# Optimization experiments

Hardware: AMD Instinct MI355X
Metric: run time of the kernel (lower is better)

The kernel has to match this reference:

```python
import jax, jax.numpy as jnp
import numpy as np

B, S, D, H = 2, 2048, 2048, 16
HD = D // H
DFF = 4 * D
EPS = 1e-5


def _gelu(x):
    # tanh-approximate GELU as in the torch module
    c = jnp.sqrt(jnp.asarray(2.0 / jnp.pi, dtype=x.dtype))
    return 0.5 * x * (1.0 + jnp.tanh(c * (x + 0.044715 * x ** 3)))


def _layernorm(x, scale, shift):
    mean = jnp.mean(x, axis=-1, keepdims=True)
    var = jnp.mean((x - mean) ** 2, axis=-1, keepdims=True)  # unbiased=False
    return scale * (x - mean) / jnp.sqrt(var + EPS) + shift


def setup_inputs() -> dict:
    key = jax.random.key(0)
    ks = jax.random.split(key, 8)
    std = 0.02
    return {
        "x": jax.random.normal(ks[0], (B, S, D), dtype=jnp.float32),
        "Wq": std * jax.random.normal(ks[1], (D, D), dtype=jnp.float32),
        "Wk": std * jax.random.normal(ks[2], (D, D), dtype=jnp.float32),
        "Wv": std * jax.random.normal(ks[3], (D, D), dtype=jnp.float32),
        "Wo": std * jax.random.normal(ks[4], (D, D), dtype=jnp.float32),
        "bo": jnp.zeros((D,), dtype=jnp.float32),
        "ln1_scale": jnp.ones((D,), dtype=jnp.float32),
        "ln1_shift": jnp.zeros((D,), dtype=jnp.float32),
        "ln2_scale": jnp.ones((D,), dtype=jnp.float32),
        "ln2_shift": jnp.zeros((D,), dtype=jnp.float32),
        "W1": std * jax.random.normal(ks[5], (D, DFF), dtype=jnp.float32),
        "b1": jnp.zeros((DFF,), dtype=jnp.float32),
        "W2": std * jax.random.normal(ks[6], (DFF, D), dtype=jnp.float32),
        "b2": jnp.zeros((D,), dtype=jnp.float32),
    }


def _attention(x, Wq, Wk, Wv, Wo, bo):
    b, s, d = x.shape
    q = (x @ Wq).reshape(b, s, H, HD).transpose(0, 2, 1, 3)  # bhsd
    k = (x @ Wk).reshape(b, s, H, HD).transpose(0, 2, 1, 3)
    v = (x @ Wv).reshape(b, s, H, HD).transpose(0, 2, 1, 3)
    scores = jnp.einsum("bhqd,bhkd->bhqk", q, k)
    causal = jnp.tril(jnp.ones((s, s), dtype=bool))
    scores = jnp.where(causal, scores, -jnp.inf)
    w = jax.nn.softmax(scores / jnp.sqrt(jnp.asarray(HD, dtype=x.dtype)), axis=-1)
    ctx = jnp.einsum("bhqk,bhkd->bhqd", w, v)
    ctx = ctx.transpose(0, 2, 1, 3).reshape(b, s, d)
    return ctx @ Wo + bo


def reference(x, Wq, Wk, Wv, Wo, bo, ln1_scale, ln1_shift, ln2_scale, ln2_shift, W1, b1, W2, b2):
    # pre-LN transformer block; dropout rate 0 -> identity
    h = x + _attention(_layernorm(x, ln1_scale, ln1_shift), Wq, Wk, Wv, Wo, bo)
    y = _gelu(_layernorm(h, ln2_scale, ln2_shift) @ W1 + b1)
    return h + (y @ W2 + b2)
```

## Files before the change

### kernel.cpp

```cpp
#include <hip/hip_runtime.h>
#include <cmath>


typedef unsigned short u16;
typedef unsigned int   u32;
typedef float  f32x4   __attribute__((ext_vector_type(4)));
typedef short  s16x8   __attribute__((ext_vector_type(8)));
typedef short  s16x4   __attribute__((ext_vector_type(4)));
typedef __bf16 bf16x8  __attribute__((ext_vector_type(8)));

#define DEV __device__ __forceinline__

DEV u16 f2bf(float f) {
  union { float f; u32 u; } v; v.f = f;
  u32 u = v.u;
  u += 0x7fffu + ((u >> 16) & 1u);
  return (u16)(u >> 16);
}

DEV f32x4 mfma16(s16x8 a, s16x8 b, f32x4 c) {
  return __builtin_amdgcn_mfma_f32_16x16x32_bf16(
      __builtin_bit_cast(bf16x8, a), __builtin_bit_cast(bf16x8, b), c, 0, 0, 0);
}

DEV float gelu_f(float x) {
  const float c = 0.7978845608028654f;
  const float z = c * (x + 0.044715f * x * x * x);
  const float e = __expf(2.0f * z);
  const float th = 1.0f - 2.0f / (e + 1.0f);
  return 0.5f * x * (1.0f + th);
}

DEV void gload16(const u16* g, u16* l) {
  __builtin_amdgcn_global_load_lds(
      (const __attribute__((address_space(1))) u32*)(const void*)g,
      (__attribute__((address_space(3))) u32*)(void*)l, 16, 0, 0);
}

__global__ __launch_bounds__(256) void transpose_cast(
    const float* __restrict__ W, u16* __restrict__ Wt, int K, int N) {
  __shared__ float tile[32][33];
  const int n0 = blockIdx.x * 32, k0 = blockIdx.y * 32;
  const int tx = threadIdx.x, ty = threadIdx.y;
#pragma unroll
  for (int i = 0; i < 4; ++i)
    tile[ty + 8 * i][tx] = W[(size_t)(k0 + ty + 8 * i) * N + n0 + tx];
  __syncthreads();
#pragma unroll
  for (int i = 0; i < 4; ++i)
    Wt[(size_t)(n0 + ty + 8 * i) * K + k0 + tx] = f2bf(tile[tx][ty + 8 * i]);
}

__global__ __launch_bounds__(256) void transpose_v(
    const u16* __restrict__ QKV, u16* __restrict__ VT) {
  __shared__ u16 tile[32][33];
  const int s0 = blockIdx.x * 32;
  const int d0 = blockIdx.y * 32;
  const int bh = blockIdx.z;
  const int b = bh >> 4, h = bh & 15;
  const int tx = threadIdx.x, ty = threadIdx.y;
  const u16* src = QKV + (long)b * 2048 * 6144 + 4096 + h * 128;
#pragma unroll
  for (int i = 0; i < 4; ++i)
    tile[ty + 8 * i][tx] = src[(long)(s0 + ty + 8 * i) * 6144 + d0 + tx];
  __syncthreads();
  u16* dst = VT + (long)bh * 128 * 2048;
#pragma unroll
  for (int i = 0; i < 4; ++i)
    dst[(long)(d0 + ty + 8 * i) * 2048 + s0 + tx] = tile[tx][ty + 8 * i];
}

__global__ __launch_bounds__(256) void ln_kernel(
    const float* __restrict__ X, const float* __restrict__ sc,
    const float* __restrict__ sh, u16* __restrict__ Y) {
  const int row = blockIdx.x, t = threadIdx.x;
  const float* xr = X + (size_t)row * 2048;
  float4 v0 = ((const float4*)xr)[t];
  float4 v1 = ((const float4*)xr)[t + 256];
  float s  = v0.x + v0.y + v0.z + v0.w + v1.x + v1.y + v1.z + v1.w;
  float qs = v0.x*v0.x + v0.y*v0.y + v0.z*v0.z + v0.w*v0.w
           + v1.x*v1.x + v1.y*v1.y + v1.z*v1.z + v1.w*v1.w;
#pragma unroll
  for (int off = 1; off < 64; off <<= 1) {
    s  += __shfl_xor(s, off);
    qs += __shfl_xor(qs, off);
  }
  __shared__ float rs[4], rq[4];
  if ((t & 63) == 0) { rs[t >> 6] = s; rq[t >> 6] = qs; }
  __syncthreads();
  const float st = rs[0] + rs[1] + rs[2] + rs[3];
  const float qt = rq[0] + rq[1] + rq[2] + rq[3];
  const float mean = st * (1.0f / 2048.0f);
  const float var  = qt * (1.0f / 2048.0f) - mean * mean;
  const float rstd = rsqrtf(var + 1e-5f);

  u16* yr = Y + (size_t)row * 2048;
  const int c0 = t * 4, c1 = 1024 + t * 4;
  s16x4 o0, o1;
  o0[0] = (short)f2bf(sc[c0+0] * (v0.x - mean) * rstd + sh[c0+0]);
  o0[1] = (short)f2bf(sc[c0+1] * (v0.y - mean) * rstd + sh[c0+1]);
  o0[2] = (short)f2bf(sc[c0+2] * (v0.z - mean) * rstd + sh[c0+2]);
  o0[3] = (short)f2bf(sc[c0+3] * (v0.w - mean) * rstd + sh[c0+3]);
  o1[0] = (short)f2bf(sc[c1+0] * (v1.x - mean) * rstd + sh[c1+0]);
  o1[1] = (short)f2bf(sc[c1+1] * (v1.y - mean) * rstd + sh[c1+1]);
  o1[2] = (short)f2bf(sc[c1+2] * (v1.z - mean) * rstd + sh[c1+2]);
  o1[3] = (short)f2bf(sc[c1+3] * (v1.w - mean) * rstd + sh[c1+3]);
  *(s16x4*)(yr + c0) = o0;
  *(s16x4*)(yr + c1) = o1;
}

template<int MHALF, int STORE_BF16, int BIAS, int RES, int GELU_ACT>
__global__ __launch_bounds__(512, 2) void gemm8(
    const u16* __restrict__ A, const u16* __restrict__ Bt,
    const float* __restrict__ bias, const float* __restrict__ res,
    float* __restrict__ Cf, u16* __restrict__ Cb,
    int M, int N, int K, int rr, int rc) {
  constexpr int NPH   = 2 * MHALF;
  constexpr int ABUFS = (MHALF == 2) ? 2 : 3;
  constexpr int ASZ   = 8192 * MHALF;
  constexpr int BOFF  = ABUFS * ASZ;
  __shared__ u16 lds[BOFF + 2 * 16384];

  const int t9 = threadIdx.x;
  const int l = t9 & 63, w = t9 >> 6;
  const int r16 = l & 15, quad = l >> 4;
  const int wm = w >> 2, wn = w & 3;

  const int nbx = N >> 8;
  const int bid = blockIdx.x;
  const int xcd = bid & 7, j = bid >> 3;
  const int nregc = nbx / rc;
  const int m_t = (xcd / nregc) * rr + (j % rr);
  const int n_t = (xcd % nregc) * rc + (j / rr);
  const long m0 = (long)m_t * (128 * MHALF);
  const long n0 = (long)n_t * 256;

  const int NT = K >> 6;
  const int srow = t9 >> 3;
  const int scol = (t9 & 7) ^ (srow & 7);

  const u16* Abase = A  + (m0 + srow) * (long)K + scol * 8;
  const u16* Bbase = Bt + (n0 + srow) * (long)K + scol * 8;
  const long rowK64  = 64 * (long)K;
  const long rowK128 = 128 * (long)K;

  #define STAGE_A(tile, h) { \
    u16* d = &lds[((tile) % ABUFS) * ASZ + (h) * 8192 + w * 512]; \
    const u16* s = Abase + (h) * rowK128 + (long)(tile) * 64; \
    gload16(s, d); gload16(s + rowK64, d + 4096); }
  #define STAGE_B(tile, h) { \
    u16* d = &lds[BOFF + ((tile) & 1) * 16384 + (h) * 8192 + w * 512]; \
    const u16* s = Bbase + (h) * rowK128 + (long)(tile) * 64; \
    gload16(s, d); gload16(s + rowK64, d + 4096); }

  f32x4 acc[4 * MHALF][4] = {};

  if (MHALF == 2) {
    STAGE_B(0, 0); STAGE_B(0, 1); STAGE_A(0, 0); STAGE_A(0, 1);
    STAGE_B(1, 0); STAGE_B(1, 1);
    asm volatile("s_waitcnt vmcnt(4)" ::: "memory");
  } else {
    STAGE_B(0, 0); STAGE_B(0, 1); STAGE_A(0, 0); STAGE_A(1, 0);
    STAGE_B(1, 0); STAGE_B(1, 1);
    asm volatile("s_waitcnt vmcnt(6)" ::: "memory");
  }
  __builtin_amdgcn_sched_barrier(0);
  __builtin_amdgcn_s_barrier();

  s16x8 bf_[4][2];
  for (int t = 0; t < NT; ++t) {
    const int ab = t % ABUFS;
    const u16* Abuf = &lds[ab * ASZ];
    const u16* Bbuf = &lds[BOFF + (t & 1) * 16384];
#pragma unroll
    for (int p = 0; p < NPH; ++p) {
      if (p == 0) {
#pragma unroll
        for (int ni = 0; ni < 4; ++ni) {
          const int brow = wn * 64 + ni * 16 + r16;
#pragma unroll
          for (int ks = 0; ks < 2; ++ks)
            bf_[ni][ks] = *(const s16x8*)&Bbuf[brow * 64 + ((ks * 4 + quad) ^ (brow & 7)) * 8];
        }
      }
      s16x8 af[2][2];
#pragma unroll
      for (int mi = 0; mi < 2; ++mi) {
        const int arow = (MHALF == 2 ? wm * 128 : wm * 64) + (2 * p + mi) * 16 + r16;
#pragma unroll
        for (int ks = 0; ks < 2; ++ks)
          af[mi][ks] = *(const s16x8*)&Abuf[arow * 64 + ((ks * 4 + quad) ^ (arow & 7)) * 8];
      }
      if (MHALF == 2) {
        if (p < 2)       { if (t + 1 < NT) STAGE_A(t + 1, p); }
        else             { if (t + 2 < NT) STAGE_B(t + 2, p - 2); }
      } else {
        if (p == 0)      { if (t + 2 < NT) STAGE_A(t + 2, 0); }
        else             { if (t + 2 < NT) { STAGE_B(t + 2, 0); STAGE_B(t + 2, 1); } }
      }
      __builtin_amdgcn_sched_barrier(0);
      __builtin_amdgcn_s_barrier();
      asm volatile("s_waitcnt lgkmcnt(0)" ::: "memory");
      __builtin_amdgcn_sched_barrier(0);
      __builtin_amdgcn_s_setprio(1);
#pragma unroll
      for (int mi = 0; mi < 2; ++mi)
#pragma unroll
        for (int ni = 0; ni < 4; ++ni)
#pragma unroll
          for (int ks = 0; ks < 2; ++ks)
            acc[2 * p + mi][ni] = mfma16(af[mi][ks], bf_[ni][ks], acc[2 * p + mi][ni]);
      __builtin_amdgcn_s_setprio(0);
      __builtin_amdgcn_sched_barrier(0);
      if (p == NPH - 1) {
        if (MHALF == 2) {
          if (t + 2 < NT) { asm volatile("s_waitcnt vmcnt(4)" ::: "memory"); }
          else            { asm volatile("s_waitcnt vmcnt(0)" ::: "memory"); }
        } else {
          if (t + 2 < NT) { asm volatile("s_waitcnt vmcnt(6)" ::: "memory"); }
          else            { asm volatile("s_waitcnt vmcnt(0)" ::: "memory"); }
        }
        __builtin_amdgcn_sched_barrier(0);
      }
      __builtin_amdgcn_s_barrier();
    }
  }
  #undef STAGE_A
  #undef STAGE_B

#pragma unroll
  for (int mi = 0; mi < 4 * MHALF; ++mi) {
#pragma unroll
    for (int ni = 0; ni < 4; ++ni) {
#pragma unroll
      for (int r = 0; r < 4; ++r) {
        const long gr = m0 + (MHALF == 2 ? wm * 128 : wm * 64) + mi * 16 + quad * 4 + r;
        const long gc = n0 + wn * 64 + ni * 16 + r16;
        float v = acc[mi][ni][r];
        if (BIAS)     v += bias[gc];
        if (GELU_ACT) v  = gelu_f(v);
        if (RES)      v += res[gr * N + gc];
        if (STORE_BF16) Cb[gr * N + gc] = f2bf(v);
        else            Cf[gr * N + gc] = v;
      }
    }
  }
}

__global__ __launch_bounds__(512) void attn_kernel(
    const u16* __restrict__ QKV, const u16* __restrict__ VT,
    u16* __restrict__ CTX) {
  __shared__ u16 Ks[2][64 * 128];
  __shared__ u16 Vs[2][128 * 64];
  __shared__ u16 Pl[8][16 * 64];

  const int t = threadIdx.x;
  const int lane = t & 63, w = t >> 6;
  const int r16 = lane & 15, quad = lane >> 4;
  const int h = blockIdx.y, b = blockIdx.z;
  const long LDQ = 6144;
  const u16* Qb = QKV + (long)b * 2048 * LDQ + h * 128;
  const u16* Kb = Qb + 2048;
  const u16* Vtb = VT + (long)(b * 16 + h) * 128 * 2048;
  u16* Pw = Pl[w];
  const float scale = 0.08838834764831845f;

  const int k_r = w * 4 + (lane >> 4);
  const int k_s = lane & 15;
  const int v_r = w * 8 + (lane >> 3);
  const int v_s = lane & 7;

#define STAGE_KV(kt_, buf_)                                                    \
  {                                                                            \
    const int kb_ = (kt_) * 64;                                                \
    _Pragma("unroll") for (int i = 0; i < 2; ++i) {                            \
      const int row = i * 32 + k_r;                                            \
      gload16(Kb + (long)(kb_ + row) * LDQ + (k_s ^ (row & 7)) * 8,            \
              &Ks[buf_][i * 4096 + w * 512]);                                  \
    }                                                                          \
    _Pragma("unroll") for (int i = 0; i < 2; ++i) {                            \
      const int d_ = i * 64 + v_r;                                             \
      gload16(Vtb + (long)d_ * 2048 + kb_ + (v_s ^ (d_ & 7)) * 8,              \
              &Vs[buf_][i * 4096 + w * 512]);                                  \
    }                                                                          \
  }

  for (int half = 0; half < 2; ++half) {
    const int qt = half ? (15 - (int)blockIdx.x) : (int)blockIdx.x;
    const int qw = qt * 128 + w * 16;

    s16x8 aq[4];
#pragma unroll
    for (int ks = 0; ks < 4; ++ks)
      aq[ks] = *(const s16x8*)(Qb + (long)(qw + r16) * LDQ + ks * 32 + quad * 8);

    f32x4 o[8] = {};
    float mrun[4], lrun[4];
#pragma unroll
    for (int r = 0; r < 4; ++r) { mrun[r] = -1e30f; lrun[r] = 0.0f; }

    __builtin_amdgcn_s_barrier();
    STAGE_KV(0, 0);
    asm volatile("s_waitcnt vmcnt(0)" ::: "memory");
    __builtin_amdgcn_s_barrier();

    const int nkt = 2 * qt + 2;
    for (int kt = 0; kt < nkt; ++kt) {
      const int kbase = kt * 64;
      const int cur = kt & 1;
      if (kt + 1 < nkt) STAGE_KV(kt + 1, cur ^ 1);

      if (kbase <= qw + 15) {
        f32x4 sc[4];
#pragma unroll
        for (int kh = 0; kh < 4; ++kh) {
          f32x4 z = {};
          sc[kh] = z;
          const int krow = kh * 16 + r16;
#pragma unroll
          for (int ks = 0; ks < 4; ++ks) {
            const s16x8 bk =
                *(const s16x8*)&Ks[cur][krow * 128 + ((ks * 4 + quad) ^ (krow & 7)) * 8];
            sc[kh] = mfma16(aq[ks], bk, sc[kh]);
          }
        }
        const bool need_mask = (kbase + 63 > qw);
        float alpha[4];
#pragma unroll
        for (int r = 0; r < 4; ++r) {
          const int q = qw + quad * 4 + r;
          float sv[4];
#pragma unroll
          for (int kh = 0; kh < 4; ++kh) {
            float s = sc[kh][r] * scale;
            if (need_mask && (kbase + kh * 16 + r16 > q)) s = -1e30f;
            sv[kh] = s;
          }
          float mx = fmaxf(fmaxf(sv[0], sv[1]), fmaxf(sv[2], sv[3]));
#pragma unroll
          for (int off = 1; off < 16; off <<= 1) mx = fmaxf(mx, __shfl_xor(mx, off));
          const float mn = fmaxf(mrun[r], mx);
          alpha[r] = __expf(mrun[r] - mn);
          mrun[r] = mn;
          const int prow = quad * 4 + r;
          float ps = 0.0f;
#pragma unroll
          for (int kh = 0; kh < 4; ++kh) {
            const float p = __expf(sv[kh] - mn);
            ps += p;
            Pw[(prow * 64 + kh * 16 + r16) ^ ((prow & 7) << 3)] = f2bf(p);
          }
          lrun[r] = lrun[r] * alpha[r] + ps;
        }
        if (alpha[0] != 1.0f || alpha[1] != 1.0f || alpha[2] != 1.0f || alpha[3] != 1.0f) {
#pragma unroll
          for (int ds = 0; ds < 8; ++ds)
#pragma unroll
            for (int r = 0; r < 4; ++r) o[ds][r] *= alpha[r];
        }
#pragma unroll
        for (int s = 0; s < 2; ++s) {
          const s16x8 ap =
              *(const s16x8*)&Pw[(r16 * 64 + s * 32 + quad * 8) ^ ((r16 & 7) << 3)];
#pragma unroll
          for (int ds = 0; ds < 8; ++ds) {
            const int d = ds * 16 + r16;
            const s16x8 bv =
                *(const s16x8*)&Vs[cur][d * 64 + ((s * 4 + quad) ^ (d & 7)) * 8];
            o[ds] = mfma16(ap, bv, o[ds]);
          }
        }
      }

      asm volatile("s_waitcnt vmcnt(0)" ::: "memory");
      __builtin_amdgcn_s_barrier();
    }

#pragma unroll
    for (int r = 0; r < 4; ++r)
#pragma unroll
      for (int off = 1; off < 16; off <<= 1) lrun[r] += __shfl_xor(lrun[r], off);

#pragma unroll
    for (int ds = 0; ds < 8; ++ds)
#pragma unroll
      for (int r = 0; r < 4; ++r) {
        const float v = o[ds][r] / lrun[r];
        CTX[(long)(b * 2048 + qw + quad * 4 + r) * 2048 + h * 128 + ds * 16 + r16] = f2bf(v);
      }
  }
#undef STAGE_KV
}

extern "C" void kernel_launch(void* const* d_in, const int* in_sizes, int n_in,
                              void* d_out, int out_size, void* d_ws, size_t ws_size,
                              hipStream_t stream) {
  (void)in_sizes; (void)n_in; (void)out_size; (void)ws_size;
  const float* x    = (const float*)d_in[0];
  const float* Wq   = (const float*)d_in[1];
  const float* Wk   = (const float*)d_in[2];
  const float* Wv   = (const float*)d_in[3];
  const float* Wo   = (const float*)d_in[4];
  const float* bo   = (const float*)d_in[5];
  const float* ln1s = (const float*)d_in[6];
  const float* ln1b = (const float*)d_in[7];
  const float* ln2s = (const float*)d_in[8];
  const float* ln2b = (const float*)d_in[9];
  const float* W1   = (const float*)d_in[10];
  const float* b1   = (const float*)d_in[11];
  const float* W2   = (const float*)d_in[12];
  const float* b2   = (const float*)d_in[13];
  float* out = (float*)d_out;

  const int Mtok = 4096, D = 2048, DFF = 8192, NQKV = 6144;

  char* w = (char*)d_ws;
  u16* Wt_qkv = (u16*)w;  w += (size_t)NQKV * D * 2;
  u16* Wt_o   = (u16*)w;  w += (size_t)D * D * 2;
  u16* Wt_1   = (u16*)w;  w += (size_t)DFF * D * 2;
  u16* Wt_2   = (u16*)w;  w += (size_t)D * DFF * 2;
  u16* Xln    = (u16*)w;  w += (size_t)Mtok * D * 2;
  u16* QKV    = (u16*)w;  w += (size_t)Mtok * NQKV * 2;
  u16* CTX    = (u16*)w;  w += (size_t)Mtok * D * 2;
  u16* Y1     = QKV;
  u16* VTb    = Wt_qkv;
  float* Hbuf = (float*)w; w += (size_t)Mtok * D * 4;

  const dim3 tb(32, 8, 1);
  transpose_cast<<<dim3(D / 32, D / 32), tb, 0, stream>>>(Wq, Wt_qkv,                    D, D);
  transpose_cast<<<dim3(D / 32, D / 32), tb, 0, stream>>>(Wk, Wt_qkv + (size_t)D * D,    D, D);
  transpose_cast<<<dim3(D / 32, D / 32), tb, 0, stream>>>(Wv, Wt_qkv + (size_t)2 * D * D,D, D);
  transpose_cast<<<dim3(D / 32, D / 32), tb, 0, stream>>>(Wo, Wt_o,                      D, D);
  transpose_cast<<<dim3(DFF / 32, D / 32), tb, 0, stream>>>(W1, Wt_1,                    D, DFF);
  transpose_cast<<<dim3(D / 32, DFF / 32), tb, 0, stream>>>(W2, Wt_2,                    DFF, D);

  ln_kernel<<<Mtok, 256, 0, stream>>>(x, ln1s, ln1b, Xln);

  gemm8<1, 1, 0, 0, 0><<<dim3(768), 512, 0, stream>>>(
      Xln, Wt_qkv, nullptr, nullptr, nullptr, QKV, Mtok, NQKV, D, 16, 6);

  transpose_v<<<dim3(64, 4, 32), tb, 0, stream>>>(QKV, VTb);

  attn_kernel<<<dim3(8, 16, 2), 512, 0, stream>>>(QKV, VTb, CTX);

  gemm8<1, 0, 1, 1, 0><<<dim3(256), 512, 0, stream>>>(
      CTX, Wt_o, bo, x, Hbuf, nullptr, Mtok, D, D, 8, 4);

  ln_kernel<<<Mtok, 256, 0, stream>>>(Hbuf, ln2s, ln2b, Xln);

  gemm8<2, 1, 1, 0, 1><<<dim3(512), 512, 0, stream>>>(
      Xln, Wt_1, b1, nullptr, nullptr, Y1, Mtok, DFF, D, 8, 8);

  gemm8<1, 0, 1, 1, 0><<<dim3(256), 512, 0, stream>>>(
      Y1, Wt_2, b2, Hbuf, out, nullptr, Mtok, D, DFF, 8, 4);
}
```

Before: 637.2 us.

## Add 256x256 phased GEMM kernel and split-K FFN down-projection

Introduces a new 256x256-tile GEMM kernel with double-buffered LDS, XOR-swizzled loads, and four interleaved MFMA phases with priority hints. It replaces the W1 GEMM and the W2 GEMM. The W2 GEMM is split along K into two halves, writing partials to out and to a scratch buffer that reuses the W1 weight workspace, and a separate reduce kernel adds the partials, bias and residual. This targets better reuse and enough CTAs for the N=2048 down-projection, at the cost of an extra fp32 partial round-trip and an additional kernel launch.

```diff
diff --git a/kernel.cpp b/kernel.cpp
--- a/kernel.cpp
+++ b/kernel.cpp
@@ -244,6 +244,187 @@
         else            Cf[gr * N + gc] = v;
       }
     }
+  }
+}
+
+template<int SPLITK, int STORE_BF16, int BIAS, int GELU_ACT>
+__global__ __launch_bounds__(512, 2) void gemm256(
+    const u16* __restrict__ A, const u16* __restrict__ Bt,
+    const float* __restrict__ bias,
+    float* __restrict__ Cf, u16* __restrict__ Cb, float* __restrict__ Cf2,
+    int M, int N, int K, int rr, int rc) {
+  __shared__ u16 ldsA[2 * 16384];
+  __shared__ u16 ldsB[2 * 16384];
+
+  const int t9 = threadIdx.x;
+  const int l = t9 & 63, w = t9 >> 6;
+  const int r16 = l & 15, quad = l >> 4;
+  const int wm = w >> 2, wn = w & 3;
+
+  const int nbx = N >> 8;
+  const int bid = blockIdx.x;
+  const int xcd = bid & 7, j = bid >> 3;
+  const int j2 = SPLITK ? (j >> 1) : j;
+  const int kh = SPLITK ? (j & 1) : 0;
+  const int nregc = nbx / rc;
+  const int m_t = (xcd / nregc) * rr + (j2 % rr);
+  const int n_t = (xcd % nregc) * rc + (j2 / rr);
+  const long m0 = (long)m_t * 256;
+  const long n0 = (long)n_t * 256;
+
+  const int Klen = SPLITK ? (K >> 1) : K;
+  const long koff = (long)kh * Klen;
+  const int NT = Klen >> 6;
+
+  const int srow = t9 >> 3;
+  const int scol = (t9 & 7) ^ (srow & 7);
+
+  const u16* Abase = A  + (m0 + srow) * (long)K + koff + scol * 8;
+  const u16* Bbase = Bt + (n0 + srow) * (long)K + koff + scol * 8;
+  const long rowK64 = 64 * (long)K;
+
+  #define SA(tile, c) gload16(Abase + (c) * rowK64 + (long)(tile) * 64, \
+                              &ldsA[((tile) & 1) * 16384 + (c) * 4096 + w * 512])
+  #define SB(tile, c) gload16(Bbase + (c) * rowK64 + (long)(tile) * 64, \
+                              &ldsB[((tile) & 1) * 16384 + (c) * 4096 + w * 512])
+
+  f32x4 acc[8][4] = {};
+
+  SB(0, 0); SB(0, 1); SB(0, 2); SB(0, 3);
+  SA(0, 0); SA(0, 1); SA(0, 2); SA(0, 3);
+  SB(1, 0); SB(1, 1); SB(1, 2); SB(1, 3);
+  asm volatile("s_waitcnt vmcnt(4)" ::: "memory");
+  __builtin_amdgcn_sched_barrier(0);
+  __builtin_amdgcn_s_barrier();
+
+  #define PH_BEGIN \
+    __builtin_amdgcn_sched_barrier(0); \
+    __builtin_amdgcn_s_barrier(); \
+    asm volatile("s_waitcnt lgkmcnt(0)" ::: "memory"); \
+    __builtin_amdgcn_sched_barrier(0); \
+    __builtin_amdgcn_s_setprio(1);
+  #define PH_END \
+    __builtin_amdgcn_s_setprio(0); \
+    __builtin_amdgcn_sched_barrier(0);
+
+  for (int t = 0; t < NT; ++t) {
+    const u16* Abuf = &ldsA[(t & 1) * 16384];
+    const u16* Bbuf = &ldsB[(t & 1) * 16384];
+    const bool preA = (t + 1 < NT);
+    const bool preB = (t + 2 < NT);
+    s16x8 bfk[4], af[4];
+
+#pragma unroll
+    for (int ni = 0; ni < 4; ++ni) {
+      const int br = wn * 64 + ni * 16 + r16;
+      bfk[ni] = *(const s16x8*)&Bbuf[br * 64 + (quad ^ (br & 7)) * 8];
+    }
+#pragma unroll
+    for (int mi = 0; mi < 4; ++mi) {
+      const int ar = wm * 128 + mi * 16 + r16;
+      af[mi] = *(const s16x8*)&Abuf[ar * 64 + (quad ^ (ar & 7)) * 8];
+    }
+    if (preA) { SA(t + 1, 0); SA(t + 1, 1); }
+    PH_BEGIN
+#pragma unroll
+    for (int mi = 0; mi < 4; ++mi)
+#pragma unroll
+      for (int ni = 0; ni < 4; ++ni)
+        acc[mi][ni] = mfma16(af[mi], bfk[ni], acc[mi][ni]);
+    PH_END
+    __builtin_amdgcn_s_barrier();
+
+#pragma unroll
+    for (int mi = 0; mi < 4; ++mi) {
+      const int ar = wm * 128 + (4 + mi) * 16 + r16;
+      af[mi] = *(const s16x8*)&Abuf[ar * 64 + (quad ^ (ar & 7)) * 8];
+    }
+    if (preA) { SA(t + 1, 2); SA(t + 1, 3); }
+    PH_BEGIN
+#pragma unroll
+    for (int mi = 0; mi < 4; ++mi)
+#pragma unroll
+      for (int ni = 0; ni < 4; ++ni)
+        acc[4 + mi][ni] = mfma16(af[mi], bfk[ni], acc[4 + mi][ni]);
+    PH_END
+    __builtin_amdgcn_s_barrier();
+
+#pragma unroll
+    for (int ni = 0; ni < 4; ++ni) {
+      const int br = wn * 64 + ni * 16 + r16;
+      bfk[ni] = *(const s16x8*)&Bbuf[br * 64 + ((4 + quad) ^ (br & 7)) * 8];
+    }
+#pragma unroll
+    for (int mi = 0; mi < 4; ++mi) {
+      const int ar = wm * 128 + mi * 16 + r16;
+      af[mi] = *(const s16x8*)&Abuf[ar * 64 + ((4 + quad) ^ (ar & 7)) * 8];
+    }
+    PH_BEGIN
+#pragma unroll
+    for (int mi = 0; mi < 4; ++mi)
+#pragma unroll
+      for (int ni = 0; ni < 4; ++ni)
+        acc[mi][ni] = mfma16(af[mi], bfk[ni], acc[mi][ni]);
+    PH_END
+    __builtin_amdgcn_s_barrier();
+
+#pragma unroll
+    for (int mi = 0; mi < 4; ++mi) {
+      const int ar = wm * 128 + (4 + mi) * 16 + r16;
+      af[mi] = *(const s16x8*)&Abuf[ar * 64 + ((4 + quad) ^ (ar & 7)) * 8];
+    }
+    if (preB) { SB(t + 2, 0); SB(t + 2, 1); SB(t + 2, 2); SB(t + 2, 3); }
+    PH_BEGIN
+#pragma unroll
+    for (int mi = 0; mi < 4; ++mi)
+#pragma unroll
+      for (int ni = 0; ni < 4; ++ni)
+        acc[4 + mi][ni] = mfma16(af[mi], bfk[ni], acc[4 + mi][ni]);
+    PH_END
+    if (preB)      { asm volatile("s_waitcnt vmcnt(4)" ::: "memory"); }
+    else if (preA) { asm volatile("s_waitcnt vmcnt(0)" ::: "memory"); }
+    __builtin_amdgcn_sched_barrier(0);
+    __builtin_amdgcn_s_barrier();
+  }
+  #undef SA
+  #undef SB
+  #undef PH_BEGIN
+  #undef PH_END
+
+  float* dstf = (SPLITK && kh) ? Cf2 : Cf;
+#pragma unroll
+  for (int mi = 0; mi < 8; ++mi) {
+#pragma unroll
+    for (int ni = 0; ni < 4; ++ni) {
+#pragma unroll
+      for (int r = 0; r < 4; ++r) {
+        const long gr = m0 + wm * 128 + mi * 16 + quad * 4 + r;
+        const long gc = n0 + wn * 64 + ni * 16 + r16;
+        float v = acc[mi][ni][r];
+        if (BIAS)     v += bias[gc];
+        if (GELU_ACT) v  = gelu_f(v);
+        if (STORE_BF16) Cb[gr * N + gc] = f2bf(v);
+        else            dstf[gr * N + gc] = v;
+      }
+    }
+  }
+}
+
+__global__ __launch_bounds__(256) void splitk_reduce(
+    const float* __restrict__ p1, const float* __restrict__ res,
+    const float* __restrict__ bias, float* __restrict__ out, int N, long nf4) {
+  const long stride = (long)gridDim.x * 256;
+  for (long i = blockIdx.x * 256 + threadIdx.x; i < nf4; i += stride) {
+    float4 a = ((const float4*)out)[i];
+    float4 b = ((const float4*)p1)[i];
+    float4 r = ((const float4*)res)[i];
+    const int col = (int)((i * 4) % N);
+    float4 bb = *(const float4*)&bias[col];
+    a.x += b.x + r.x + bb.x;
+    a.y += b.y + r.y + bb.y;
+    a.z += b.z + r.z + bb.z;
+    a.w += b.w + r.w + bb.w;
+    ((float4*)out)[i] = a;
   }
 }
 
@@ -424,6 +605,7 @@
   u16* CTX    = (u16*)w;  w += (size_t)Mtok * D * 2;
   u16* Y1     = QKV;
   u16* VTb    = Wt_qkv;
+  float* P1   = (float*)Wt_1;
   float* Hbuf = (float*)w; w += (size_t)Mtok * D * 4;
 
   const dim3 tb(32, 8, 1);
@@ -448,9 +630,12 @@
 
   ln_kernel<<<Mtok, 256, 0, stream>>>(Hbuf, ln2s, ln2b, Xln);
 
-  gemm8<2, 1, 1, 0, 1><<<dim3(512), 512, 0, stream>>>(
-      Xln, Wt_1, b1, nullptr, nullptr, Y1, Mtok, DFF, D, 8, 8);
-
-  gemm8<1, 0, 1, 1, 0><<<dim3(256), 512, 0, stream>>>(
-      Y1, Wt_2, b2, Hbuf, out, nullptr, Mtok, D, DFF, 8, 4);
-}
+  gemm256<0, 1, 1, 1><<<dim3(512), 512, 0, stream>>>(
+      Xln, Wt_1, b1, nullptr, Y1, nullptr, Mtok, DFF, D, 8, 8);
+
+  gemm256<1, 0, 0, 0><<<dim3(256), 512, 0, stream>>>(
+      Y1, Wt_2, nullptr, out, nullptr, P1, Mtok, D, DFF, 4, 4);
+
+  splitk_reduce<<<dim3(2048), 256, 0, stream>>>(
+      P1, Hbuf, b2, out, D, (long)Mtok * D / 4);
+}
```

Result: slower. 676.8 us (+6.2%).
